# Performance work log

Measured on AMD Instinct MI355X. Metric: run time of the kernel, lower is better.

Reference implementation:

```python
import jax, jax.numpy as jnp
import numpy as np


def setup_inputs() -> dict:
    key = jax.random.key(0)
    W0 = jax.random.normal(key, (8192, 8192), dtype=jnp.float32)
    return {"W0": W0}


def reference(W0) -> jnp.ndarray:
    # Faithful to the torch code: elementwise exp (NOT matrix_exp), then trace.
    if W0.ndim == 3 and W0.shape[2] == 1:
        W0 = W0[:, :, 0]
    N = W0.shape[0]
    # trace(exp(W*W)) only touches the diagonal after elementwise exp,
    # but we compute the full elementwise map as the original does; the
    # mathematically equivalent reduced form is sum(exp(diag(W)**2)).
    tr = jnp.trace(jnp.exp(W0 * W0))
    return (tr - N) ** 2.0
```

## Files before the change

kernel.cpp:

```cpp
#include <hip/hip_runtime.h>
#include <math.h>


__global__ __launch_bounds__(1024) void diag_trace_loss_kernel(
    const float* __restrict__ W, float* __restrict__ out, int N) {
    const int tid = threadIdx.x;
    const size_t stride = (size_t)N + 1;

    double acc = 0.0;
    for (int i = tid; i < N; i += 1024) {
        float x = W[(size_t)i * stride];
        acc += (double)expf(x * x);
    }

    #pragma unroll
    for (int off = 32; off > 0; off >>= 1)
        acc += __shfl_down(acc, off, 64);

    __shared__ double wave_sums[16];
    const int lane = tid & 63;
    const int wave = tid >> 6;
    if (lane == 0) wave_sums[wave] = acc;
    __syncthreads();

    if (wave == 0) {
        double v = (lane < 16) ? wave_sums[lane] : 0.0;
        #pragma unroll
        for (int off = 8; off > 0; off >>= 1)
            v += __shfl_down(v, off, 64);
        if (lane == 0) {
            double d = v - (double)N;
            out[0] = (float)(d * d);
        }
    }
}

extern "C" void kernel_launch(void* const* d_in, const int* in_sizes, int n_in,
                              void* d_out, int out_size, void* d_ws, size_t ws_size,
                              hipStream_t stream) {
    const float* W = (const float*)d_in[0];
    float* out = (float*)d_out;

    long long total = (long long)in_sizes[0];
    int N = (int)(sqrt((double)total) + 0.5);

    diag_trace_loss_kernel<<<1, 1024, 0, stream>>>(W, out, N);
}
```

Baseline: 10.20 us.

## Split diagonal trace reduction into multi-block partial sums plus final kernel

Replaces the single 1024-thread block with 128 single-wave blocks, each reading 64 diagonal elements and writing a double partial sum to workspace. A second one-wave kernel then reduces the partials and computes the squared loss. This spreads the strided, latency-bound diagonal loads across many CUs, at the cost of a second kernel launch and a round trip through global memory.

```diff
diff --git a/kernel.cpp b/kernel.cpp
--- a/kernel.cpp
+++ b/kernel.cpp
@@ -2,36 +2,40 @@
 #include <math.h>
 
 
-__global__ __launch_bounds__(1024) void diag_trace_loss_kernel(
-    const float* __restrict__ W, float* __restrict__ out, int N) {
-    const int tid = threadIdx.x;
+__global__ __launch_bounds__(64) void diag_partial_kernel(
+    const float* __restrict__ W, double* __restrict__ partials, int N) {
+    const int lane = threadIdx.x;
+    const int i = blockIdx.x * 64 + lane;
     const size_t stride = (size_t)N + 1;
 
     double acc = 0.0;
-    for (int i = tid; i < N; i += 1024) {
+    if (i < N) {
         float x = W[(size_t)i * stride];
-        acc += (double)expf(x * x);
+        acc = (double)expf(x * x);
     }
 
     #pragma unroll
     for (int off = 32; off > 0; off >>= 1)
         acc += __shfl_down(acc, off, 64);
 
-    __shared__ double wave_sums[16];
-    const int lane = tid & 63;
-    const int wave = tid >> 6;
-    if (lane == 0) wave_sums[wave] = acc;
-    __syncthreads();
+    if (lane == 0) partials[blockIdx.x] = acc;
+}
 
-    if (wave == 0) {
-        double v = (lane < 16) ? wave_sums[lane] : 0.0;
-        #pragma unroll
-        for (int off = 8; off > 0; off >>= 1)
-            v += __shfl_down(v, off, 64);
-        if (lane == 0) {
-            double d = v - (double)N;
-            out[0] = (float)(d * d);
-        }
+__global__ __launch_bounds__(64) void diag_final_kernel(
+    const double* __restrict__ partials, float* __restrict__ out,
+    int nparts, int N) {
+    const int lane = threadIdx.x;
+    double acc = 0.0;
+    for (int p = lane; p < nparts; p += 64)
+        acc += partials[p];
+
+    #pragma unroll
+    for (int off = 32; off > 0; off >>= 1)
+        acc += __shfl_down(acc, off, 64);
+
+    if (lane == 0) {
+        double d = acc - (double)N;
+        out[0] = (float)(d * d);
     }
 }
 
@@ -40,9 +44,12 @@
                               hipStream_t stream) {
     const float* W = (const float*)d_in[0];
     float* out = (float*)d_out;
+    double* partials = (double*)d_ws;
 
     long long total = (long long)in_sizes[0];
     int N = (int)(sqrt((double)total) + 0.5);
 
-    diag_trace_loss_kernel<<<1, 1024, 0, stream>>>(W, out, N);
+    int nblocks = (N + 63) / 64;
+    diag_partial_kernel<<<nblocks, 64, 0, stream>>>(W, partials, N);
+    diag_final_kernel<<<1, 64, 0, stream>>>(partials, out, nblocks, N);
 }
```

Measured after the change: 11.55 us. 13.3% more time.
